# Performance work log

Hardware: AMD Instinct MI355X
Metric: run time of the kernel (lower is better)

## Reference

```python
import jax, jax.numpy as jnp
import numpy as np

B, V, P, D = 32, 6, 197, 512
L = 77          # CLIP token length
C = 5           # num quality perspectives (conditions)

def _normalize(x, axis=-1, eps=1e-12):
    n = jnp.linalg.norm(x, axis=axis, keepdims=True)
    return x / jnp.maximum(n, eps)

def _conv3x3(x, w, b):
    # x: [C,112,7,7], w: [O,112,3,3] -> [C,O,7,7]
    y = jax.lax.conv_general_dilated(x, w, (1, 1), 'SAME',
                                     dimension_numbers=('NCHW', 'OIHW', 'NCHW'))
    return y + b[None, :, None, None]

def setup_inputs() -> dict:
    key = jax.random.key(0)
    ks = jax.random.split(key, 20)
    s = 0.02  # weight init scale keeps sigmoids in linear-ish range
    return {
        'feature_texture': jax.random.normal(ks[0], (B, V * P, D), jnp.float32),
        'feature_prompt': jax.random.normal(ks[1], (B, L, D), jnp.float32),
        'feature_prompt_eot': jax.random.normal(ks[2], (B, D), jnp.float32),
        'feature_condition': jax.random.normal(ks[3], (C, D), jnp.float32),
        'fc_quality_w': jax.random.normal(ks[4], (224, D), jnp.float32) * s,
        'fc_quality_b': jnp.zeros((224,), jnp.float32),
        'fc_condition_w': jax.random.normal(ks[5], (5488, D), jnp.float32) * s,
        'fc_condition_b': jnp.zeros((5488,), jnp.float32),
        'fc1w_conv_w': jax.random.normal(ks[6], (512, 112, 3, 3), jnp.float32) * s,
        'fc1w_conv_b': jnp.zeros((512,), jnp.float32),
        'fc2w_conv_w': jax.random.normal(ks[7], (128, 112, 3, 3), jnp.float32) * s,
        'fc2w_conv_b': jnp.zeros((128,), jnp.float32),
        'fc3w_conv_w': jax.random.normal(ks[8], (32, 112, 3, 3), jnp.float32) * s,
        'fc3w_conv_b': jnp.zeros((32,), jnp.float32),
        'fc4w_conv_w': jax.random.normal(ks[9], (8, 112, 3, 3), jnp.float32) * s,
        'fc4w_conv_b': jnp.zeros((8,), jnp.float32),
        'fc1b_w': jax.random.normal(ks[10], (112, 112), jnp.float32) * s,
        'fc1b_b': jnp.zeros((112,), jnp.float32),
        'fc2b_w': jax.random.normal(ks[11], (56, 112), jnp.float32) * s,
        'fc2b_b': jnp.zeros((56,), jnp.float32),
        'fc3b_w': jax.random.normal(ks[12], (28, 112), jnp.float32) * s,
        'fc3b_b': jnp.zeros((28,), jnp.float32),
        'fc4b_w': jax.random.normal(ks[13], (14, 112), jnp.float32) * s,
        'fc4b_b': jnp.zeros((14,), jnp.float32),
        'fc5w_w': jax.random.normal(ks[14], (14, 112), jnp.float32) * s,
        'fc5w_b': jnp.zeros((14,), jnp.float32),
        'fc5b_w': jax.random.normal(ks[15], (1, 112), jnp.float32) * s,
        'fc5b_b': jnp.zeros((1,), jnp.float32),
    }

def reference(feature_texture, feature_prompt, feature_prompt_eot, feature_condition,
              fc_quality_w, fc_quality_b, fc_condition_w, fc_condition_b,
              fc1w_conv_w, fc1w_conv_b, fc2w_conv_w, fc2w_conv_b,
              fc3w_conv_w, fc3w_conv_b, fc4w_conv_w, fc4w_conv_b,
              fc1b_w, fc1b_b, fc2b_w, fc2b_b, fc3b_w, fc3b_b, fc4b_w, fc4b_b,
              fc5w_w, fc5w_b, fc5b_w, fc5b_b):
    nC = feature_condition.shape[0]

    # --- calculate_cos: mean of relu(pairwise cosine sim), upper triangle i<j ---
    fn = _normalize(feature_condition)                      # [C,512]
    gram = fn @ fn.T                                        # [C,C]
    iu, ju = jnp.triu_indices(nC, k=1)
    loss_dis = jnp.mean(jnp.maximum(gram[iu, ju], 0.0))

    # --- cross-attention-style patch weighting ---
    np_prompt = _normalize(feature_prompt, axis=2)          # [B,L,D]
    np_tex = _normalize(feature_texture, axis=2)            # [B,J,D]
    sim_texture = jnp.einsum('bid,bjd->bji', np_prompt, np_tex)   # [B,J,L]
    sim_cond = jnp.einsum('bid,cd->bci', np_prompt, fn)           # [B,C,L]
    patch_weight = jnp.einsum('bcl,bjl->bjc', sim_cond, sim_texture)  # [B,J,C]
    patch_weight = jax.nn.softmax(patch_weight, axis=1)

    # --- condition feature maps for hypernet: [C,112,7,7] ---
    cond_maps = (feature_condition @ fc_condition_w.T + fc_condition_b)
    cond_maps = cond_maps.reshape(nC, 112, 7, 7)

    # --- hypernet: generate TargetNet params for all conditions at once ---
    pooled = cond_maps.mean(axis=(2, 3))                              # [C,112]
    fc1w = _conv3x3(cond_maps, fc1w_conv_w, fc1w_conv_b).reshape(nC, 112, 224)
    fc2w = _conv3x3(cond_maps, fc2w_conv_w, fc2w_conv_b).reshape(nC, 56, 112)
    fc3w = _conv3x3(cond_maps, fc3w_conv_w, fc3w_conv_b).reshape(nC, 28, 56)
    fc4w = _conv3x3(cond_maps, fc4w_conv_w, fc4w_conv_b).reshape(nC, 14, 28)
    fc1b = pooled @ fc1b_w.T + fc1b_b                                 # [C,112]
    fc2b = pooled @ fc2b_w.T + fc2b_b                                 # [C,56]
    fc3b = pooled @ fc3b_w.T + fc3b_b                                 # [C,28]
    fc4b = pooled @ fc4b_w.T + fc4b_b                                 # [C,14]
    fc5w = pooled @ fc5w_w.T + fc5w_b                                 # [C,14]
    fc5b = pooled @ fc5b_w.T + fc5b_b                                 # [C,1]

    # --- fused quality feature per (batch, condition) ---
    ftf = jnp.einsum('bjd,bjc->bcd', feature_texture, patch_weight)   # [B,C,D]
    fused = ftf * feature_prompt_eot[:, None, :]                      # [B,C,D]
    fq = jnp.einsum('bcd,kd->bck', fused, fc_quality_w) + fc_quality_b  # [B,C,224]

    # --- TargetNet (per-condition generated weights), vectorized over loop ---
    h = jax.nn.sigmoid(jnp.einsum('bck,cjk->bcj', fq, fc1w) + fc1b[None])
    h = jax.nn.sigmoid(jnp.einsum('bcj,cij->bci', h, fc2w) + fc2b[None])
    h = jax.nn.sigmoid(jnp.einsum('bci,coi->bco', h, fc3w) + fc3b[None])
    h = jax.nn.sigmoid(jnp.einsum('bco,cpo->bcp', h, fc4w) + fc4b[None])
    score_list = jnp.einsum('bcp,cp->bc', h, fc5w) + fc5b[:, 0][None]  # [B,C]

    return score_list, loss_dis
```

## Files before the change

kernel.cpp:

```cpp
#include <hip/hip_runtime.h>
#include <hip/hip_bf16.h>
#include <math.h>

#define B_   32
#define J_   1182
#define D_   512
#define L_   77
#define C_   5
#define JC_  64
#define NCH_ 19
#define NPW_ 37

__device__ __forceinline__ float dot4(float4 a, float4 b) {
    return a.x*b.x + a.y*b.y + a.z*b.z + a.w*b.w;
}

__device__ __forceinline__ float wave_sum(float v) {
#pragma unroll
    for (int off = 32; off > 0; off >>= 1) v += __shfl_xor(v, off, 64);
    return v;
}

__device__ __forceinline__ float wave_max(float v) {
#pragma unroll
    for (int off = 32; off > 0; off >>= 1) v = fmaxf(v, __shfl_xor(v, off, 64));
    return v;
}

__global__ void k_front(const float* __restrict__ fc, const float* __restrict__ cw,
                        const float* __restrict__ cb, float* __restrict__ cm,
                        float* __restrict__ loss_out,
                        const float* __restrict__ fp, float* __restrict__ swl) {
    __shared__ float4 smem4[640];
    float* sfc = (float*)smem4;
    int bid = blockIdx.x, t = threadIdx.x;
    int wave = t >> 6, lane = t & 63;

    if (bid < 1373) {
        for (int i = t; i < C_*D_; i += 256) sfc[i] = fc[i];
        __syncthreads();

        if (bid == 1372) {
            for (int c = wave; c < C_; c += 4) {
                float ss = 0.f;
                for (int d = lane; d < D_; d += 64) { float v = sfc[c*D_+d]; ss += v*v; }
                ss = wave_sum(ss);
                float inv = 1.f / fmaxf(sqrtf(ss), 1e-12f);
                for (int d = lane; d < D_; d += 64) sfc[c*D_+d] *= inv;
            }
            __syncthreads();
            if (wave == 0) {
                float acc = 0.f;
                for (int i = 0; i < C_; ++i)
                    for (int j = i+1; j < C_; ++j) {
                        float p = 0.f;
                        for (int d = lane; d < D_; d += 64) p += sfc[i*D_+d]*sfc[j*D_+d];
                        p = wave_sum(p);
                        acc += fmaxf(p, 0.f);
                    }
                if (lane == 0) *loss_out = acc * (1.f/10.f);
            }
            return;
        }

        int o = bid*4 + wave;
        const float4* w4 = (const float4*)(cw + (size_t)o*D_);
        float4 wa = w4[lane], wb = w4[lane+64];
        float bias = cb[o];
        float keep = 0.f;
#pragma unroll
        for (int c = 0; c < C_; ++c) {
            const float4* f4 = (const float4*)(sfc + c*D_);
            float s = dot4(wa, f4[lane]) + dot4(wb, f4[lane+64]);
            s = wave_sum(s);
            if (lane == c) keep = s;
        }
        if (lane < C_) cm[lane*5488 + o] = keep + bias;
        return;
    }

    for (int c = wave; c < C_; c += 4) {
        const float4* f8 = (const float4*)(fc + c*D_);
        float4 v0 = f8[lane*2], v1 = f8[lane*2+1];
        float ss = dot4(v0,v0) + dot4(v1,v1);
        ss = wave_sum(ss);
        float inv = 1.f / fmaxf(sqrtf(ss), 1e-12f);
        v0.x*=inv; v0.y*=inv; v0.z*=inv; v0.w*=inv;
        v1.x*=inv; v1.y*=inv; v1.z*=inv; v1.w*=inv;
        int f0 = lane*2, f1 = lane*2+1;
        smem4[(c*16 + (f0 & 15))*8 + (f0 >> 4)] = v0;
        smem4[(c*16 + (f1 & 15))*8 + (f1 >> 4)] = v1;
    }
    __syncthreads();

    int row = t >> 3, seg = t & 7;
    int bl = (bid - 1373)*32 + row;
    int b = bl / L_, l = bl - b*L_;
    const float4* p4 = ((const float4*)(fp + (size_t)bl*D_)) + seg*16;
    float ss=0.f, s0=0.f, s1=0.f, s2=0.f, s3=0.f, s4=0.f;
#pragma unroll 4
    for (int k = 0; k < 16; ++k) {
        float4 v = p4[k];
        int base = k*8 + seg;
        ss += dot4(v, v);
        s0 += dot4(v, smem4[base]);
        s1 += dot4(v, smem4[128 + base]);
        s2 += dot4(v, smem4[256 + base]);
        s3 += dot4(v, smem4[384 + base]);
        s4 += dot4(v, smem4[512 + base]);
    }
#pragma unroll
    for (int off = 1; off < 8; off <<= 1) {
        ss += __shfl_xor(ss,off,64);
        s0 += __shfl_xor(s0,off,64); s1 += __shfl_xor(s1,off,64);
        s2 += __shfl_xor(s2,off,64); s3 += __shfl_xor(s3,off,64);
        s4 += __shfl_xor(s4,off,64);
    }
    if (seg == 0) {
        float inv = 1.f / fmaxf(sqrtf(ss), 1e-12f);
        float inv2 = inv*inv;
        swl[((size_t)(b*C_+0))*L_ + l] = s0*inv2;
        swl[((size_t)(b*C_+1))*L_ + l] = s1*inv2;
        swl[((size_t)(b*C_+2))*L_ + l] = s2*inv2;
        swl[((size_t)(b*C_+3))*L_ + l] = s3*inv2;
        swl[((size_t)(b*C_+4))*L_ + l] = s4*inv2;
    }
}

__global__ void k_Q(const float* __restrict__ fp, const float* __restrict__ swl,
                    float* __restrict__ Q) {
    __shared__ float sw[C_][80];
    int b = blockIdx.y;
    int t = threadIdx.x;
    for (int i = t; i < C_*L_; i += 256) { int c = i/L_, l = i - c*L_; sw[c][l] = swl[((size_t)(b*C_+c))*L_ + l]; }
    __syncthreads();
    int d = blockIdx.x*256 + t;
    float a0=0.f, a1=0.f, a2=0.f, a3=0.f, a4=0.f;
    const float* f = fp + (size_t)b*L_*D_ + d;
    for (int l = 0; l < L_; ++l) {
        float v = f[(size_t)l*D_];
        a0 += sw[0][l]*v; a1 += sw[1][l]*v; a2 += sw[2][l]*v;
        a3 += sw[3][l]*v; a4 += sw[4][l]*v;
    }
    Q[(size_t)(b*C_+0)*D_ + d] = a0;
    Q[(size_t)(b*C_+1)*D_ + d] = a1;
    Q[(size_t)(b*C_+2)*D_ + d] = a2;
    Q[(size_t)(b*C_+3)*D_ + d] = a3;
    Q[(size_t)(b*C_+4)*D_ + d] = a4;
}

__global__ void k_conv_pw(const float* __restrict__ cm,
                          const float* __restrict__ w1, const float* __restrict__ bb1,
                          const float* __restrict__ w2, const float* __restrict__ bb2,
                          const float* __restrict__ w3, const float* __restrict__ bb3,
                          const float* __restrict__ w4, const float* __restrict__ bb4,
                          float* __restrict__ o1, float* __restrict__ o2,
                          float* __restrict__ o3, float* __restrict__ o4,
                          const float* __restrict__ w1b, const float* __restrict__ b1b,
                          const float* __restrict__ w2b, const float* __restrict__ b2b,
                          const float* __restrict__ w3b, const float* __restrict__ b3b,
                          const float* __restrict__ w4b, const float* __restrict__ b4b,
                          const float* __restrict__ w5w, const float* __restrict__ b5w,
                          const float* __restrict__ w5b, const float* __restrict__ b5b,
                          float* __restrict__ fcb,
                          const float* __restrict__ tex, const float* __restrict__ Q,
                          float* __restrict__ pw, float2* __restrict__ pstat) {
    __shared__ float4 smem4[3052];
    int bid = blockIdx.x;
    int t = threadIdx.x;

    if (bid >= 375) {
        float4* qs = smem4;
        float* sraw = (float*)(smem4 + 640);
        int p = bid - 375;
        int bx = p % NPW_, b = p / NPW_;
        {
            const float4* q4 = (const float4*)(Q + (size_t)b*C_*D_);
            for (int i = t; i < C_*128; i += 256) {
                int c = i >> 7, f = i & 127;
                qs[(c*16 + (f & 15))*8 + (f >> 4)] = q4[i];
            }
        }
        __syncthreads();
        int row = t >> 3, seg = t & 7;
        int j = bx*32 + row;
        bool valid = (j < J_);
        int jc = valid ? j : (J_-1);
        const float4* tp = (const float4*)(tex + ((size_t)(b*J_ + jc))*D_ + seg*64);
        float ss=0.f, s0=0.f, s1=0.f, s2=0.f, s3=0.f, s4=0.f;
#pragma unroll 4
        for (int k = 0; k < 16; ++k) {
            float4 v = tp[k];
            int base = k*8 + seg;
            ss += dot4(v, v);
            s0 += dot4(v, qs[base]);
            s1 += dot4(v, qs[128 + base]);
            s2 += dot4(v, qs[256 + base]);
            s3 += dot4(v, qs[384 + base]);
            s4 += dot4(v, qs[512 + base]);
        }
#pragma unroll
        for (int off = 1; off < 8; off <<= 1) {
            ss += __shfl_xor(ss,off,64);
            s0 += __shfl_xor(s0,off,64); s1 += __shfl_xor(s1,off,64);
            s2 += __shfl_xor(s2,off,64); s3 += __shfl_xor(s3,off,64);
            s4 += __shfl_xor(s4,off,64);
        }
        if (seg == 0) {
            float inv = 1.f / fmaxf(sqrtf(ss), 1e-12f);
            float r0 = s0*inv, r1 = s1*inv, r2 = s2*inv, r3 = s3*inv, r4 = s4*inv;
            if (valid) {
                pw[((size_t)(b*C_+0))*J_ + j] = r0;
                pw[((size_t)(b*C_+1))*J_ + j] = r1;
                pw[((size_t)(b*C_+2))*J_ + j] = r2;
                pw[((size_t)(b*C_+3))*J_ + j] = r3;
                pw[((size_t)(b*C_+4))*J_ + j] = r4;
                sraw[0*32+row]=r0; sraw[1*32+row]=r1; sraw[2*32+row]=r2;
                sraw[3*32+row]=r3; sraw[4*32+row]=r4;
            } else {
                sraw[0*32+row]=-1e30f; sraw[1*32+row]=-1e30f; sraw[2*32+row]=-1e30f;
                sraw[3*32+row]=-1e30f; sraw[4*32+row]=-1e30f;
            }
        }
        __syncthreads();
        if (t < C_*32) {
            int c = t >> 5, r2 = t & 31;
            float v = sraw[c*32 + r2];
            float m = v;
#pragma unroll
            for (int off = 1; off < 32; off <<= 1) m = fmaxf(m, __shfl_xor(m,off,32));
            float e = (v > -1e29f) ? expf(v - m) : 0.f;
#pragma unroll
            for (int off = 1; off < 32; off <<= 1) e += __shfl_xor(e,off,32);
            if (r2 == 0) pstat[(size_t)(bx*B_ + b)*C_ + c] = make_float2(m, e);
        }
        return;
    }

    float* im = (float*)smem4;
    float* sp = im + 12096;
    int c  = bid / 75;
    int bx = bid - c*75;
    for (int i = t; i < 112*108; i += 256) im[i] = 0.f;
    __syncthreads();
    const float* cmc = cm + c*5488;
    for (int i = t; i < 112*49; i += 256) {
        int ch = i / 49, yx = i - ch*49;
        int y = yx / 7, x = yx - y*7;
        im[ch*108 + (y+1)*12 + (x+1)] = cmc[i];
    }
    __syncthreads();

    int oy  = bx*64 + (t >> 2);
    int chq = t & 3;
    if (oy < 4760) {
        int o_comb = oy / 7, y = oy - o_comb*7;
        const float* w; const float* bias; float* outp; int o;
        if      (o_comb < 512) { w=w1; bias=bb1; outp=o1 + (size_t)c*512*49; o=o_comb; }
        else if (o_comb < 640) { w=w2; bias=bb2; outp=o2 + (size_t)c*128*49; o=o_comb-512; }
        else if (o_comb < 672) { w=w3; bias=bb3; outp=o3 + (size_t)c*32*49;  o=o_comb-640; }
        else                   { w=w4; bias=bb4; outp=o4 + (size_t)c*8*49;   o=o_comb-672; }

        float ac0=0,ac1=0,ac2=0,ac3=0,ac4=0,ac5=0,ac6=0;
        const float* wbase = w + ((size_t)o*112 + chq*28)*9;
        const float* imc   = im + (chq*28)*108 + y*12;
#pragma unroll 2
        for (int ch = 0; ch < 28; ++ch) {
            const float* wk = wbase + ch*9;
            const float* ii = imc + ch*108;
            float w0=wk[0],w1_=wk[1],w2_=wk[2],w3_=wk[3],w4_=wk[4],w5_=wk[5],w6_=wk[6],w7_=wk[7],w8_=wk[8];
#pragma unroll
            for (int ky = 0; ky < 3; ++ky) {
                const float* row = ii + ky*12;
                float4 ra = *(const float4*)(row);
                float4 rb = *(const float4*)(row + 4);
                float  rc = row[8];
                float r0=ra.x,r1=ra.y,r2=ra.z,r3=ra.w,r4=rb.x,r5=rb.y,r6=rb.z,r7=rb.w,r8=rc;
                float wk0 = (ky==0)?w0:((ky==1)?w3_:w6_);
                float wk1 = (ky==0)?w1_:((ky==1)?w4_:w7_);
                float wk2 = (ky==0)?w2_:((ky==1)?w5_:w8_);
                ac0 += r0*wk0 + r1*wk1 + r2*wk2;
                ac1 += r1*wk0 + r2*wk1 + r3*wk2;
                ac2 += r2*wk0 + r3*wk1 + r4*wk2;
                ac3 += r3*wk0 + r4*wk1 + r5*wk2;
                ac4 += r4*wk0 + r5*wk1 + r6*wk2;
                ac5 += r5*wk0 + r6*wk1 + r7*wk2;
                ac6 += r6*wk0 + r7*wk1 + r8*wk2;
            }
        }
        ac0 += __shfl_xor(ac0,1,64); ac0 += __shfl_xor(ac0,2,64);
        ac1 += __shfl_xor(ac1,1,64); ac1 += __shfl_xor(ac1,2,64);
        ac2 += __shfl_xor(ac2,1,64); ac2 += __shfl_xor(ac2,2,64);
        ac3 += __shfl_xor(ac3,1,64); ac3 += __shfl_xor(ac3,2,64);
        ac4 += __shfl_xor(ac4,1,64); ac4 += __shfl_xor(ac4,2,64);
        ac5 += __shfl_xor(ac5,1,64); ac5 += __shfl_xor(ac5,2,64);
        ac6 += __shfl_xor(ac6,1,64); ac6 += __shfl_xor(ac6,2,64);
        if (chq == 0) {
            float bo = bias[o];
            float* dst = outp + o*49 + y*7;
            dst[0]=ac0+bo; dst[1]=ac1+bo; dst[2]=ac2+bo; dst[3]=ac3+bo;
            dst[4]=ac4+bo; dst[5]=ac5+bo; dst[6]=ac6+bo;
        }
    }

    if (bx == 0) {
        if (t < 112) {
            const float* p = im + t*108;
            float s = 0.f;
            for (int k = 0; k < 108; ++k) s += p[k];
            sp[t] = s * (1.f/49.f);
        }
        __syncthreads();
        if (t < 225) {
            int rel = t;
            const float* w; const float* bb; int nout; int base;
            if      (rel < 112) {            w=w1b; bb=b1b; nout=112; base=0; }
            else if (rel < 168) { rel-=112;  w=w2b; bb=b2b; nout=56;  base=560; }
            else if (rel < 196) { rel-=168;  w=w3b; bb=b3b; nout=28;  base=840; }
            else if (rel < 210) { rel-=196;  w=w4b; bb=b4b; nout=14;  base=980; }
            else if (rel < 224) { rel-=210;  w=w5w; bb=b5w; nout=14;  base=1050; }
            else                { rel-=224;  w=w5b; bb=b5b; nout=1;   base=1120; }
            float s = bb[rel];
            const float* wr = w + rel*112;
            for (int i = 0; i < 112; ++i) s += sp[i]*wr[i];
            fcb[base + c*nout + rel] = s;
        }
    }
}

__global__ void k_ftf(const float* __restrict__ tex, const float* __restrict__ pwraw,
                      const float2* __restrict__ pstat, float* __restrict__ part) {
    __shared__ float sw[C_][JC_];
    __shared__ float2 sL[C_];
    int chunk = blockIdx.x, b = blockIdx.y;
    int t = threadIdx.x;
    int wave = t >> 6, lane = t & 63;
    if (wave < C_) {
        float2 pv = (lane < NPW_) ? pstat[(size_t)(lane*B_ + b)*C_ + wave]
                                  : make_float2(-1e30f, 0.f);
        float m = wave_max(pv.x);
        float contrib = (lane < NPW_) ? pv.y * expf(pv.x - m) : 0.f;
        float denom = wave_sum(contrib);
        if (lane == 0) sL[wave] = make_float2(m, 1.f/denom);
    }
    __syncthreads();
    int j0 = chunk*JC_;
    int jn = min(JC_, J_ - j0);
    if (t < C_*JC_) {
        int c = t >> 6, jj = t & 63;
        float2 ms = sL[c];
        sw[c][jj] = (jj < jn)
            ? expf(pwraw[((size_t)(b*C_+c))*J_ + j0 + jj] - ms.x) * ms.y
            : 0.f;
    }
    __syncthreads();
    float acc0=0.f, acc1=0.f, acc2=0.f, acc3=0.f, acc4=0.f;
    const float* tp = tex + ((size_t)b*J_ + j0)*D_ + t;
    for (int jj = 0; jj < jn; ++jj) {
        float v = tp[(size_t)jj*D_];
        acc0 += v*sw[0][jj]; acc1 += v*sw[1][jj]; acc2 += v*sw[2][jj];
        acc3 += v*sw[3][jj]; acc4 += v*sw[4][jj];
    }
    size_t base = (((size_t)chunk*B_ + b)*C_)*D_ + t;
    part[base               ] = acc0;
    part[base +   (size_t)D_] = acc1;
    part[base + 2*(size_t)D_] = acc2;
    part[base + 3*(size_t)D_] = acc3;
    part[base + 4*(size_t)D_] = acc4;
}

__global__ void k_fq_target(const float* __restrict__ part, const float* __restrict__ eot,
                            const float* __restrict__ qw, const float* __restrict__ qb,
                            const float* __restrict__ g1w, const float* __restrict__ g2w,
                            const float* __restrict__ g3w, const float* __restrict__ g4w,
                            const float* __restrict__ fcb, float* __restrict__ out) {
    int bc = blockIdx.x; int b = bc / C_; int c = bc - b*C_;
    __shared__ float sf[D_];
    __shared__ float sa[224], sb[112];
    int t = threadIdx.x;

    float s0 = 0.f, s1 = 0.f;
    for (int ch = 0; ch < NCH_; ++ch) {
        const float* p = part + ((size_t)ch*(B_*C_) + bc)*D_;
        s0 += p[t]; s1 += p[t+256];
    }
    sf[t]     = s0 * eot[b*D_ + t];
    sf[t+256] = s1 * eot[b*D_ + t + 256];
    __syncthreads();

    if (t < 224) {
        const float4* w4 = (const float4*)(qw + (size_t)t*D_);
        const float4* s4 = (const float4*)sf;
        float acc = 0.f;
#pragma unroll 4
        for (int i = 0; i < 128; ++i) acc += dot4(s4[i], w4[i]);
        sa[t] = acc + qb[t];
    }
    __syncthreads();

    if (t < 112) {
        const float* w = g1w + (size_t)c*25088 + t*224;
        float s = fcb[c*112 + t];
        for (int k = 0; k < 224; ++k) s += w[k]*sa[k];
        sb[t] = 1.f/(1.f+expf(-s));
    }
    __syncthreads();
    if (t < 56) {
        const float* w = g2w + (size_t)c*6272 + t*112;
        float s = fcb[560 + c*56 + t];
        for (int k = 0; k < 112; ++k) s += w[k]*sb[k];
        sa[t] = 1.f/(1.f+expf(-s));
    }
    __syncthreads();
    if (t < 28) {
        const float* w = g3w + (size_t)c*1568 + t*56;
        float s = fcb[840 + c*28 + t];
        for (int k = 0; k < 56; ++k) s += w[k]*sa[k];
        sb[t] = 1.f/(1.f+expf(-s));
    }
    __syncthreads();
    if (t < 14) {
        const float* w = g4w + (size_t)c*392 + t*28;
        float s = fcb[980 + c*14 + t];
        for (int k = 0; k < 28; ++k) s += w[k]*sb[k];
        sa[t] = 1.f/(1.f+expf(-s));
    }
    __syncthreads();
    if (t == 0) {
        float s = fcb[1120 + c];
        for (int p = 0; p < 14; ++p) s += sa[p]*fcb[1050 + c*14 + p];
        out[b*C_ + c] = s;
    }
}

extern "C" void kernel_launch(void* const* d_in, const int* in_sizes, int n_in,
                              void* d_out, int out_size, void* d_ws, size_t ws_size,
                              hipStream_t stream) {
    (void)in_sizes; (void)n_in; (void)out_size; (void)ws_size;
    const float* tex   = (const float*)d_in[0];
    const float* fp    = (const float*)d_in[1];
    const float* eot   = (const float*)d_in[2];
    const float* fcond = (const float*)d_in[3];
    const float* qw    = (const float*)d_in[4];
    const float* qb    = (const float*)d_in[5];
    const float* cw    = (const float*)d_in[6];
    const float* cb    = (const float*)d_in[7];
    const float* w1c   = (const float*)d_in[8];  const float* b1c = (const float*)d_in[9];
    const float* w2c   = (const float*)d_in[10]; const float* b2c = (const float*)d_in[11];
    const float* w3c   = (const float*)d_in[12]; const float* b3c = (const float*)d_in[13];
    const float* w4c   = (const float*)d_in[14]; const float* b4c = (const float*)d_in[15];
    const float* f1bw  = (const float*)d_in[16]; const float* f1bb = (const float*)d_in[17];
    const float* f2bw  = (const float*)d_in[18]; const float* f2bb = (const float*)d_in[19];
    const float* f3bw  = (const float*)d_in[20]; const float* f3bb = (const float*)d_in[21];
    const float* f4bw  = (const float*)d_in[22]; const float* f4bb = (const float*)d_in[23];
    const float* f5ww  = (const float*)d_in[24]; const float* f5wb = (const float*)d_in[25];
    const float* f5bw  = (const float*)d_in[26]; const float* f5bb = (const float*)d_in[27];
    float* out = (float*)d_out;

    float* ws     = (float*)d_ws;
    float* Qb     = ws;
    float* pw     = Qb + 81920;
    float* part   = pw + 189120;
    float* pstat  = part + 1556480;
    float* cm     = pstat + 11840;
    float* g1w    = cm + 27440;
    float* g2w    = g1w + 125440;
    float* g3w    = g2w + 31360;
    float* g4w    = g3w + 7840;
    float* fcb    = g4w + 1960;
    float* swl    = fcb + 1125;

    k_front<<<1450, 256, 0, stream>>>(fcond, cw, cb, cm, out + B_*C_, fp, swl);
    k_Q<<<dim3(2, B_), 256, 0, stream>>>(fp, swl, Qb);
    k_conv_pw<<<1559, 256, 0, stream>>>(cm, w1c, b1c, w2c, b2c, w3c, b3c, w4c, b4c,
                                        g1w, g2w, g3w, g4w,
                                        f1bw, f1bb, f2bw, f2bb, f3bw, f3bb,
                                        f4bw, f4bb, f5ww, f5wb, f5bw, f5bb, fcb,
                                        tex, Qb, pw, (float2*)pstat);
    k_ftf<<<dim3(NCH_, B_), 512, 0, stream>>>(tex, pw, (const float2*)pstat, part);
    k_fq_target<<<B_*C_, 256, 0, stream>>>(part, eot, qw, qb,
                                           g1w, g2w, g3w, g4w, fcb, out);
}
```

Before: 98.24 us.

## Interleave conv and patch-weight blocks; split conv channels across waves with LDS reduction

Conv blocks are now interleaved one in four with the patch-weight blocks across the first 1500 block IDs, instead of all being placed first. The intent is to mix the compute-heavy conv work with the memory-heavy texture work on each CU. Inside a conv block, the four channel quarters now go to separate waves rather than adjacent lanes. Partial sums are reduced through LDS instead of shuffles, and the output stores become coalesced. This adds two extra barriers and LDS traffic, and moves sp into its own shared array.

Result: slower. 101.7 us (+3.5%).

```diff
diff --git a/kernel.cpp b/kernel.cpp
--- a/kernel.cpp
+++ b/kernel.cpp
@@ -166,13 +166,15 @@
                           const float* __restrict__ tex, const float* __restrict__ Q,
                           float* __restrict__ pw, float2* __restrict__ pstat) {
     __shared__ float4 smem4[3052];
+    __shared__ float sp[112];
     int bid = blockIdx.x;
     int t = threadIdx.x;
-
-    if (bid >= 375) {
+    bool is_conv = (bid < 1500) && ((bid & 3) == 0);
+
+    if (!is_conv) {
+        int p = (bid >= 1500) ? (bid - 375) : (bid - 1 - (bid >> 2));
         float4* qs = smem4;
         float* sraw = (float*)(smem4 + 640);
-        int p = bid - 375;
         int bx = p % NPW_, b = p / NPW_;
         {
             const float4* q4 = (const float4*)(Q + (size_t)b*C_*D_);
@@ -237,10 +239,10 @@
         return;
     }
 
+    int conv_id = bid >> 2;
     float* im = (float*)smem4;
-    float* sp = im + 12096;
-    int c  = bid / 75;
-    int bx = bid - c*75;
+    int c  = conv_id / 75;
+    int bx = conv_id - c*75;
     for (int i = t; i < 112*108; i += 256) im[i] = 0.f;
     __syncthreads();
     const float* cmc = cm + c*5488;
@@ -250,58 +252,6 @@
         im[ch*108 + (y+1)*12 + (x+1)] = cmc[i];
     }
     __syncthreads();
-
-    int oy  = bx*64 + (t >> 2);
-    int chq = t & 3;
-    if (oy < 4760) {
-        int o_comb = oy / 7, y = oy - o_comb*7;
-        const float* w; const float* bias; float* outp; int o;
-        if      (o_comb < 512) { w=w1; bias=bb1; outp=o1 + (size_t)c*512*49; o=o_comb; }
-        else if (o_comb < 640) { w=w2; bias=bb2; outp=o2 + (size_t)c*128*49; o=o_comb-512; }
-        else if (o_comb < 672) { w=w3; bias=bb3; outp=o3 + (size_t)c*32*49;  o=o_comb-640; }
-        else                   { w=w4; bias=bb4; outp=o4 + (size_t)c*8*49;   o=o_comb-672; }
-
-        float ac0=0,ac1=0,ac2=0,ac3=0,ac4=0,ac5=0,ac6=0;
-        const float* wbase = w + ((size_t)o*112 + chq*28)*9;
-        const float* imc   = im + (chq*28)*108 + y*12;
-#pragma unroll 2
-        for (int ch = 0; ch < 28; ++ch) {
-            const float* wk = wbase + ch*9;
-            const float* ii = imc + ch*108;
-            float w0=wk[0],w1_=wk[1],w2_=wk[2],w3_=wk[3],w4_=wk[4],w5_=wk[5],w6_=wk[6],w7_=wk[7],w8_=wk[8];
-#pragma unroll
-            for (int ky = 0; ky < 3; ++ky) {
-                const float* row = ii + ky*12;
-                float4 ra = *(const float4*)(row);
-                float4 rb = *(const float4*)(row + 4);
-                float  rc = row[8];
-                float r0=ra.x,r1=ra.y,r2=ra.z,r3=ra.w,r4=rb.x,r5=rb.y,r6=rb.z,r7=rb.w,r8=rc;
-                float wk0 = (ky==0)?w0:((ky==1)?w3_:w6_);
-                float wk1 = (ky==0)?w1_:((ky==1)?w4_:w7_);
-                float wk2 = (ky==0)?w2_:((ky==1)?w5_:w8_);
-                ac0 += r0*wk0 + r1*wk1 + r2*wk2;
-                ac1 += r1*wk0 + r2*wk1 + r3*wk2;
-                ac2 += r2*wk0 + r3*wk1 + r4*wk2;
-                ac3 += r3*wk0 + r4*wk1 + r5*wk2;
-                ac4 += r4*wk0 + r5*wk1 + r6*wk2;
-                ac5 += r5*wk0 + r6*wk1 + r7*wk2;
-                ac6 += r6*wk0 + r7*wk1 + r8*wk2;
-            }
-        }
-        ac0 += __shfl_xor(ac0,1,64); ac0 += __shfl_xor(ac0,2,64);
-        ac1 += __shfl_xor(ac1,1,64); ac1 += __shfl_xor(ac1,2,64);
-        ac2 += __shfl_xor(ac2,1,64); ac2 += __shfl_xor(ac2,2,64);
-        ac3 += __shfl_xor(ac3,1,64); ac3 += __shfl_xor(ac3,2,64);
-        ac4 += __shfl_xor(ac4,1,64); ac4 += __shfl_xor(ac4,2,64);
-        ac5 += __shfl_xor(ac5,1,64); ac5 += __shfl_xor(ac5,2,64);
-        ac6 += __shfl_xor(ac6,1,64); ac6 += __shfl_xor(ac6,2,64);
-        if (chq == 0) {
-            float bo = bias[o];
-            float* dst = outp + o*49 + y*7;
-            dst[0]=ac0+bo; dst[1]=ac1+bo; dst[2]=ac2+bo; dst[3]=ac3+bo;
-            dst[4]=ac4+bo; dst[5]=ac5+bo; dst[6]=ac6+bo;
-        }
-    }
 
     if (bx == 0) {
         if (t < 112) {
@@ -324,6 +274,69 @@
             const float* wr = w + rel*112;
             for (int i = 0; i < 112; ++i) s += sp[i]*wr[i];
             fcb[base + c*nout + rel] = s;
+        }
+    }
+
+    int oyl = t & 63;
+    int chq = t >> 6;
+    int oy  = bx*64 + oyl;
+    bool ovalid = (oy < 4760);
+    int oyc = ovalid ? oy : 0;
+    int o_comb = oyc / 7, y = oyc - o_comb*7;
+    const float* w; int o;
+    if      (o_comb < 512) { w=w1; o=o_comb; }
+    else if (o_comb < 640) { w=w2; o=o_comb-512; }
+    else if (o_comb < 672) { w=w3; o=o_comb-640; }
+    else                   { w=w4; o=o_comb-672; }
+
+    float ac0=0,ac1=0,ac2=0,ac3=0,ac4=0,ac5=0,ac6=0;
+    const float* wbase = w + ((size_t)o*112 + chq*28)*9;
+    const float* imc   = im + (chq*28)*108 + y*12;
+#pragma unroll 2
+    for (int ch = 0; ch < 28; ++ch) {
+        const float* wk = wbase + ch*9;
+        const float* ii = imc + ch*108;
+        float w0=wk[0],w1_=wk[1],w2_=wk[2],w3_=wk[3],w4_=wk[4],w5_=wk[5],w6_=wk[6],w7_=wk[7],w8_=wk[8];
+#pragma unroll
+        for (int ky = 0; ky < 3; ++ky) {
+            const float* row = ii + ky*12;
+            float4 ra = *(const float4*)(row);
+            float4 rb = *(const float4*)(row + 4);
+            float  rc = row[8];
+            float r0=ra.x,r1=ra.y,r2=ra.z,r3=ra.w,r4=rb.x,r5=rb.y,r6=rb.z,r7=rb.w,r8=rc;
+            float wk0 = (ky==0)?w0:((ky==1)?w3_:w6_);
+            float wk1 = (ky==0)?w1_:((ky==1)?w4_:w7_);
+            float wk2 = (ky==0)?w2_:((ky==1)?w5_:w8_);
+            ac0 += r0*wk0 + r1*wk1 + r2*wk2;
+            ac1 += r1*wk0 + r2*wk1 + r3*wk2;
+            ac2 += r2*wk0 + r3*wk1 + r4*wk2;
+            ac3 += r3*wk0 + r4*wk1 + r5*wk2;
+            ac4 += r4*wk0 + r5*wk1 + r6*wk2;
+            ac5 += r5*wk0 + r6*wk1 + r7*wk2;
+            ac6 += r6*wk0 + r7*wk1 + r8*wk2;
+        }
+    }
+    __syncthreads();
+    float* partb = im;
+    {
+        int pb = (chq*64 + oyl)*9;
+        partb[pb+0]=ac0; partb[pb+1]=ac1; partb[pb+2]=ac2; partb[pb+3]=ac3;
+        partb[pb+4]=ac4; partb[pb+5]=ac5; partb[pb+6]=ac6;
+    }
+    __syncthreads();
+    for (int i = t; i < 448; i += 256) {
+        int oyl2 = i / 7, x = i - oyl2*7;
+        int oy2 = bx*64 + oyl2;
+        if (oy2 < 4760) {
+            float s = partb[(0*64+oyl2)*9+x] + partb[(1*64+oyl2)*9+x]
+                    + partb[(2*64+oyl2)*9+x] + partb[(3*64+oyl2)*9+x];
+            int oc = oy2/7, yy = oy2 - oc*7;
+            const float* bias; float* outp; int oo;
+            if      (oc < 512) { bias=bb1; outp=o1 + (size_t)c*512*49; oo=oc; }
+            else if (oc < 640) { bias=bb2; outp=o2 + (size_t)c*128*49; oo=oc-512; }
+            else if (oc < 672) { bias=bb3; outp=o3 + (size_t)c*32*49;  oo=oc-640; }
+            else               { bias=bb4; outp=o4 + (size_t)c*8*49;   oo=oc-672; }
+            outp[oo*49 + yy*7 + x] = s + bias[oo];
         }
     }
 }
```
